# Performance work log

Measured on AMD Instinct MI355X. Metric: run time of the kernel, lower is better.

## Reference

```python
import jax, jax.numpy as jnp
import numpy as np

NUM_INPUTS = 24
FACTOR = 16
VOCAB = 1_000_000
BATCH = 8192
PAIRS = NUM_INPUTS * (NUM_INPUTS - 1) // 2  # 276
HIDDEN = 64


def setup_inputs() -> dict:
    key = jax.random.key(0)
    ks = jax.random.split(key, 8)
    inputs = jax.random.randint(ks[0], (BATCH, NUM_INPUTS), 0, VOCAB)
    s = 0.01
    w = jax.random.normal(ks[1], (VOCAB, 1), dtype=jnp.float32) * s
    v = jax.random.normal(ks[2], (VOCAB, FACTOR), dtype=jnp.float32) * s
    b = jnp.zeros((1,), dtype=jnp.float32)
    W1 = jax.random.normal(ks[3], (PAIRS, 2 * FACTOR, HIDDEN), dtype=jnp.float32) * s
    b1 = jnp.zeros((PAIRS, HIDDEN), dtype=jnp.float32)
    W2 = jax.random.normal(ks[4], (PAIRS, HIDDEN, 1), dtype=jnp.float32) * s
    b2 = jnp.zeros((PAIRS, 1), dtype=jnp.float32)
    return {"inputs": inputs, "w": w, "v": v, "b": b,
            "W1": W1, "b1": b1, "W2": W2, "b2": b2}


def reference(inputs, w, v, b, W1, b1, W2, b2):
    # pair index lists (i < j) -- static
    ii, jj = np.triu_indices(NUM_INPUTS, k=1)
    ii = jnp.asarray(ii)
    jj = jnp.asarray(jj)

    # linear term: sum of 1-dim embeddings over fields
    xw = w[inputs]                      # [B, n, 1]
    l = jnp.sum(xw, axis=(1, 2))        # [B]

    # pairwise concat of factor embeddings
    xv = v[inputs]                      # [B, n, f]
    prods = jnp.concatenate([xv[:, ii, :], xv[:, jj, :]], axis=-1)  # [B, P, 2f]
    prods = jnp.transpose(prods, (1, 0, 2))                         # [P, B, 2f]

    # per-pair stacked MLP: layer 0 relu, layer 1 identity
    h = jax.nn.relu(jnp.einsum('pbi,pio->pbo', prods, W1) + b1[:, None, :])  # [P, B, H]
    out = jnp.einsum('pbi,pio->pbo', h, W2) + b2[:, None, :]                  # [P, B, 1]

    # sum over concat of pair outputs == sum over pairs and last dim
    p = jnp.sum(out, axis=(0, 2))       # [B]

    logits = l + p + b[0]
    return jax.nn.sigmoid(logits)
```

## Files before the change

### kernel.cpp

```cpp
#include <hip/hip_runtime.h>
#include <hip/hip_bf16.h>
#include <math.h>

#define BATCH   8192
#define NFIELD  24
#define FAC     16
#define PAIRS   276
#define NSETS   24
#define SETLEN  12
#define NBB     (BATCH / 64)

typedef __attribute__((ext_vector_type(8))) __bf16 bf16x8;
typedef __attribute__((ext_vector_type(4))) float f32x4;

#define XVT_OFF   0
#define COMBO_OFF 6291456
#define PART_OFF  (COMBO_OFF + 1285632)
#define WVAL_OFF  (PART_OFF + 786432)
#define CONST_OFF (WVAL_OFF + 786432)

__global__ void prep_all(const int* __restrict__ inputs,
                         const float* __restrict__ v,
                         const float* __restrict__ w,
                         const float* __restrict__ W1,
                         const float* __restrict__ W2,
                         const float* __restrict__ b1,
                         const float* __restrict__ b2,
                         const float* __restrict__ bsc,
                         __hip_bfloat16* __restrict__ xvT,
                         char* __restrict__ combo,
                         float* __restrict__ wval,
                         float* __restrict__ consts) {
    __shared__ float red[256];
    int blk = blockIdx.x;
    if (blk < 768) {
        int t = blk * 256 + threadIdx.x;
        int field = t >> 13;
        int b = t & 8191;
        int idx = inputs[b * NFIELD + field];
        const float4* src = (const float4*)(v + (long)idx * FAC);
        union { __hip_bfloat16 h[16]; uint4 u[2]; } tmp;
        float4 a0 = src[0], a1 = src[1], a2 = src[2], a3 = src[3];
        tmp.h[0]  = __float2bfloat16(a0.x); tmp.h[1]  = __float2bfloat16(a0.y);
        tmp.h[2]  = __float2bfloat16(a0.z); tmp.h[3]  = __float2bfloat16(a0.w);
        tmp.h[4]  = __float2bfloat16(a1.x); tmp.h[5]  = __float2bfloat16(a1.y);
        tmp.h[6]  = __float2bfloat16(a1.z); tmp.h[7]  = __float2bfloat16(a1.w);
        tmp.h[8]  = __float2bfloat16(a2.x); tmp.h[9]  = __float2bfloat16(a2.y);
        tmp.h[10] = __float2bfloat16(a2.z); tmp.h[11] = __float2bfloat16(a2.w);
        tmp.h[12] = __float2bfloat16(a3.x); tmp.h[13] = __float2bfloat16(a3.y);
        tmp.h[14] = __float2bfloat16(a3.z); tmp.h[15] = __float2bfloat16(a3.w);
        int bb = b >> 6, row = b & 63;
        __hip_bfloat16* base = xvT + (long)bb * 24576 + field * 1024 + row * 8;
        *(uint4*)base         = tmp.u[0];
        *(uint4*)(base + 512) = tmp.u[1];
        wval[field * BATCH + b] = w[idx];
    } else {
        int wb = blk - 768;
        int t = wb * 256 + threadIdx.x;
        int p = t >> 6;
        int L = t & 63;
        int q = L >> 4, c = L & 15;
        char* base = combo + (long)p * 4608;
        union { __hip_bfloat16 h[8]; uint4 u; } buf;
#pragma unroll
        for (int tt = 0; tt < 4; ++tt) {
#pragma unroll
            for (int jj = 0; jj < 8; ++jj)
                buf.h[jj] = __float2bfloat16(W1[p * 2048 + (q * 8 + jj) * 64 + tt * 16 + c]);
            *(uint4*)(base + 512 + tt * 1024 + L * 16) = buf.u;
        }
        if (L < 16) {
            float4 bv = {b1[p * 64 + L], b1[p * 64 + 16 + L], b1[p * 64 + 32 + L], b1[p * 64 + 48 + L]};
            *(float4*)(base + L * 16) = bv;
            float4 wv = {W2[p * 64 + L], W2[p * 64 + 16 + L], W2[p * 64 + 32 + L], W2[p * 64 + 48 + L]};
            *(float4*)(base + 256 + L * 16) = wv;
        }
        if (wb == 1) {
            uint4 z = {0, 0, 0, 0};
            for (int k = threadIdx.x; k < 576; k += 256)
                *(uint4*)(combo + (long)PAIRS * 4608 + k * 16) = z;
        }
        if (wb == 0) {
            float s = 0.f;
            for (int k = threadIdx.x; k < PAIRS; k += 256) s += b2[k];
            red[threadIdx.x] = s;
            __syncthreads();
            for (int off = 128; off > 0; off >>= 1) {
                if (threadIdx.x < off) red[threadIdx.x] += red[threadIdx.x + off];
                __syncthreads();
            }
            if (threadIdx.x == 0) consts[0] = red[0] + bsc[0];
        }
    }
}

struct Pkg {
    f32x4 cb0, cb1, cb2, cb3;
    float4 mw;
    bf16x8 f0, f1, f2, f3;
};

__device__ __forceinline__ Pkg load_pkg(const char* p, int mcol, int l16) {
    Pkg k;
    float4 tb = *(const float4*)(p + mcol);
    k.cb0 = (f32x4){tb.x, tb.x, tb.x, tb.x};
    k.cb1 = (f32x4){tb.y, tb.y, tb.y, tb.y};
    k.cb2 = (f32x4){tb.z, tb.z, tb.z, tb.z};
    k.cb3 = (f32x4){tb.w, tb.w, tb.w, tb.w};
    k.mw = *(const float4*)(p + 256 + mcol);
    k.f0 = *(const bf16x8*)(p + 512  + l16);
    k.f1 = *(const bf16x8*)(p + 1536 + l16);
    k.f2 = *(const bf16x8*)(p + 2560 + l16);
    k.f3 = *(const bf16x8*)(p + 3584 + l16);
    return k;
}

#define PKGCOMP(P)                                                            \
    {                                                                         \
        int fso = ((quad < 2) ? i : j) * 1088;                                \
        const f32x4 z4 = {0.f, 0.f, 0.f, 0.f};                                \
        _Pragma("unroll")                                                     \
        for (int t = 0; t < 4; ++t) {                                         \
            bf16x8 af = *(const bf16x8*)(xv_s + fso + abase + t * 128);       \
            f32x4 c0 = __builtin_amdgcn_mfma_f32_16x16x32_bf16(af, P.f0, P.cb0, 0, 0, 0); \
            f32x4 c1 = __builtin_amdgcn_mfma_f32_16x16x32_bf16(af, P.f1, P.cb1, 0, 0, 0); \
            f32x4 c2 = __builtin_amdgcn_mfma_f32_16x16x32_bf16(af, P.f2, P.cb2, 0, 0, 0); \
            f32x4 c3 = __builtin_amdgcn_mfma_f32_16x16x32_bf16(af, P.f3, P.cb3, 0, 0, 0); \
            acc[t] = acc[t] + __builtin_elementwise_max(c0, z4) * P.mw.x;     \
            acc[t] = acc[t] + __builtin_elementwise_max(c1, z4) * P.mw.y;     \
            acc[t] = acc[t] + __builtin_elementwise_max(c2, z4) * P.mw.z;     \
            acc[t] = acc[t] + __builtin_elementwise_max(c3, z4) * P.mw.w;     \
        }                                                                     \
        ++j;                                                                  \
        if (j == NFIELD) { ++i; j = i + 1; }                                  \
    }

__global__ __launch_bounds__(256, 3) void ffm_main(
        const __hip_bfloat16* __restrict__ xvT,
        const char* __restrict__ combo,
        float* __restrict__ partial) {
    __shared__ __align__(16) __hip_bfloat16 xv_s[24 * 1088];

    int tid  = threadIdx.x;
    int bb   = blockIdx.x & (NBB - 1);
    int pg   = blockIdx.x >> 7;
    int lane = tid & 63;
    int wave = tid >> 6;
    int col  = lane & 15;
    int quad = lane >> 4;

    {
        const uint4* src = (const uint4*)(xvT + (long)bb * 24576);
#pragma unroll
        for (int it = 0; it < 12; ++it) {
            int ch = tid + it * 256;
            *(uint4*)(xv_s + ch * 8 + (ch >> 6) * 32) = src[ch];
        }
    }
    __syncthreads();

    int setid = pg * 4 + wave;
    f32x4 acc[4];
#pragma unroll
    for (int t = 0; t < 4; ++t) acc[t] = (f32x4){0.f, 0.f, 0.f, 0.f};

    const int abase = (quad & 1) * 544 + col * 8;
    const int mcol  = col * 16;
    const int l16   = lane * 16;

    if (setid < 23) {
        int p0 = setid * SETLEN;
        int i = 0, rem = p0;
        while (rem >= NFIELD - 1 - i) { rem -= NFIELD - 1 - i; ++i; }
        int j = i + 1 + rem;

        const char* wp = combo + (long)p0 * 4608;
        Pkg A = load_pkg(wp, mcol, l16);
        Pkg B = load_pkg(wp + 4608, mcol, l16);

#pragma unroll 2
        for (int k = 0; k < SETLEN; k += 2) {
            PKGCOMP(A)
            A = load_pkg(wp + 2 * 4608, mcol, l16);
            PKGCOMP(B)
            B = load_pkg(wp + 3 * 4608, mcol, l16);
            wp += 2 * 4608;
        }
    }

#pragma unroll
    for (int m = 1; m < 16; m <<= 1) {
#pragma unroll
        for (int t = 0; t < 4; ++t) {
#pragma unroll
            for (int r = 0; r < 4; ++r) acc[t][r] += __shfl_xor(acc[t][r], m, 64);
        }
    }
    if (col == 0) {
#pragma unroll
        for (int t = 0; t < 4; ++t) {
            f32x4 o = acc[t];
            *(f32x4*)&partial[setid * BATCH + bb * 64 + t * 16 + quad * 4] = o;
        }
    }
}

__global__ void finalize(const float* __restrict__ wval,
                         const float* __restrict__ consts,
                         const float* __restrict__ partial,
                         float* __restrict__ out) {
    int b = blockIdx.x * 256 + threadIdx.x;
    float s = consts[0];
#pragma unroll
    for (int f = 0; f < NFIELD; ++f) s += wval[f * BATCH + b];
#pragma unroll
    for (int g = 0; g < NSETS; ++g) s += partial[g * BATCH + b];
    out[b] = 1.0f / (1.0f + expf(-s));
}

extern "C" void kernel_launch(void* const* d_in, const int* in_sizes, int n_in,
                              void* d_out, int out_size, void* d_ws, size_t ws_size,
                              hipStream_t stream) {
    const int*   inputs = (const int*)d_in[0];
    const float* w      = (const float*)d_in[1];
    const float* v      = (const float*)d_in[2];
    const float* bsc    = (const float*)d_in[3];
    const float* W1     = (const float*)d_in[4];
    const float* b1     = (const float*)d_in[5];
    const float* W2     = (const float*)d_in[6];
    const float* b2     = (const float*)d_in[7];
    float* out = (float*)d_out;

    char* ws = (char*)d_ws;
    __hip_bfloat16* xvT = (__hip_bfloat16*)(ws + XVT_OFF);
    char*  combo   = ws + COMBO_OFF;
    float* partial = (float*)(ws + PART_OFF);
    float* wval    = (float*)(ws + WVAL_OFF);
    float* consts  = (float*)(ws + CONST_OFF);

    prep_all<<<768 + 69, 256, 0, stream>>>(inputs, v, w, W1, W2, b1, b2, bsc,
                                           xvT, combo, wval, consts);
    ffm_main<<<NBB * 6, 256, 0, stream>>>(xvT, combo, partial);
    finalize<<<BATCH / 256, 256, 0, stream>>>(wval, consts, partial, out);
}
```

Measured before the change: 136.5 us.

## Fuse prep, main and finalize into one cooperative kernel with grid syncs

Merges the three launches (gather/repack, per-pair MLP MFMA kernel, finalize) into a single cooperative kernel of 768 blocks that separates the phases with grid-wide syncs. The goal is to remove launch gaps and kernel-boundary drain between stages. The grid must fit co-resident (768 blocks at 3 per CU on 256 CUs). If the cooperative launch fails, the code falls back to the original three kernels. Grid syncs add their own barrier cost, and block-level load imbalance in the gather phase now stalls the whole grid.

```diff
diff --git a/kernel.cpp b/kernel.cpp
--- a/kernel.cpp
+++ b/kernel.cpp
@@ -1,6 +1,9 @@
 #include <hip/hip_runtime.h>
+#include <hip/hip_cooperative_groups.h>
 #include <hip/hip_bf16.h>
 #include <math.h>
+
+namespace cg = cooperative_groups;
 
 #define BATCH   8192
 #define NFIELD  24
@@ -19,79 +22,72 @@
 #define WVAL_OFF  (PART_OFF + 786432)
 #define CONST_OFF (WVAL_OFF + 786432)
 
-__global__ void prep_all(const int* __restrict__ inputs,
-                         const float* __restrict__ v,
-                         const float* __restrict__ w,
-                         const float* __restrict__ W1,
-                         const float* __restrict__ W2,
-                         const float* __restrict__ b1,
-                         const float* __restrict__ b2,
-                         const float* __restrict__ bsc,
-                         __hip_bfloat16* __restrict__ xvT,
-                         char* __restrict__ combo,
-                         float* __restrict__ wval,
-                         float* __restrict__ consts) {
-    __shared__ float red[256];
-    int blk = blockIdx.x;
-    if (blk < 768) {
-        int t = blk * 256 + threadIdx.x;
-        int field = t >> 13;
-        int b = t & 8191;
-        int idx = inputs[b * NFIELD + field];
-        const float4* src = (const float4*)(v + (long)idx * FAC);
-        union { __hip_bfloat16 h[16]; uint4 u[2]; } tmp;
-        float4 a0 = src[0], a1 = src[1], a2 = src[2], a3 = src[3];
-        tmp.h[0]  = __float2bfloat16(a0.x); tmp.h[1]  = __float2bfloat16(a0.y);
-        tmp.h[2]  = __float2bfloat16(a0.z); tmp.h[3]  = __float2bfloat16(a0.w);
-        tmp.h[4]  = __float2bfloat16(a1.x); tmp.h[5]  = __float2bfloat16(a1.y);
-        tmp.h[6]  = __float2bfloat16(a1.z); tmp.h[7]  = __float2bfloat16(a1.w);
-        tmp.h[8]  = __float2bfloat16(a2.x); tmp.h[9]  = __float2bfloat16(a2.y);
-        tmp.h[10] = __float2bfloat16(a2.z); tmp.h[11] = __float2bfloat16(a2.w);
-        tmp.h[12] = __float2bfloat16(a3.x); tmp.h[13] = __float2bfloat16(a3.y);
-        tmp.h[14] = __float2bfloat16(a3.z); tmp.h[15] = __float2bfloat16(a3.w);
-        int bb = b >> 6, row = b & 63;
-        __hip_bfloat16* base = xvT + (long)bb * 24576 + field * 1024 + row * 8;
-        *(uint4*)base         = tmp.u[0];
-        *(uint4*)(base + 512) = tmp.u[1];
-        wval[field * BATCH + b] = w[idx];
-    } else {
-        int wb = blk - 768;
-        int t = wb * 256 + threadIdx.x;
-        int p = t >> 6;
-        int L = t & 63;
-        int q = L >> 4, c = L & 15;
-        char* base = combo + (long)p * 4608;
-        union { __hip_bfloat16 h[8]; uint4 u; } buf;
-#pragma unroll
-        for (int tt = 0; tt < 4; ++tt) {
-#pragma unroll
-            for (int jj = 0; jj < 8; ++jj)
-                buf.h[jj] = __float2bfloat16(W1[p * 2048 + (q * 8 + jj) * 64 + tt * 16 + c]);
-            *(uint4*)(base + 512 + tt * 1024 + L * 16) = buf.u;
-        }
-        if (L < 16) {
-            float4 bv = {b1[p * 64 + L], b1[p * 64 + 16 + L], b1[p * 64 + 32 + L], b1[p * 64 + 48 + L]};
-            *(float4*)(base + L * 16) = bv;
-            float4 wv = {W2[p * 64 + L], W2[p * 64 + 16 + L], W2[p * 64 + 32 + L], W2[p * 64 + 48 + L]};
-            *(float4*)(base + 256 + L * 16) = wv;
-        }
-        if (wb == 1) {
-            uint4 z = {0, 0, 0, 0};
-            for (int k = threadIdx.x; k < 576; k += 256)
-                *(uint4*)(combo + (long)PAIRS * 4608 + k * 16) = z;
-        }
-        if (wb == 0) {
-            float s = 0.f;
-            for (int k = threadIdx.x; k < PAIRS; k += 256) s += b2[k];
-            red[threadIdx.x] = s;
-            __syncthreads();
-            for (int off = 128; off > 0; off >>= 1) {
-                if (threadIdx.x < off) red[threadIdx.x] += red[threadIdx.x + off];
-                __syncthreads();
-            }
-            if (threadIdx.x == 0) consts[0] = red[0] + bsc[0];
-        }
-    }
+
+__device__ __forceinline__ void do_gather(int blk, int tid,
+        const int* __restrict__ inputs, const float* __restrict__ v,
+        const float* __restrict__ w,
+        __hip_bfloat16* __restrict__ xvT, float* __restrict__ wval) {
+    int t = blk * 256 + tid;
+    int field = t >> 13;
+    int b = t & 8191;
+    int idx = inputs[b * NFIELD + field];
+    const float4* src = (const float4*)(v + (long)idx * FAC);
+    union { __hip_bfloat16 h[16]; uint4 u[2]; } tmp;
+    float4 a0 = src[0], a1 = src[1], a2 = src[2], a3 = src[3];
+    tmp.h[0]  = __float2bfloat16(a0.x); tmp.h[1]  = __float2bfloat16(a0.y);
+    tmp.h[2]  = __float2bfloat16(a0.z); tmp.h[3]  = __float2bfloat16(a0.w);
+    tmp.h[4]  = __float2bfloat16(a1.x); tmp.h[5]  = __float2bfloat16(a1.y);
+    tmp.h[6]  = __float2bfloat16(a1.z); tmp.h[7]  = __float2bfloat16(a1.w);
+    tmp.h[8]  = __float2bfloat16(a2.x); tmp.h[9]  = __float2bfloat16(a2.y);
+    tmp.h[10] = __float2bfloat16(a2.z); tmp.h[11] = __float2bfloat16(a2.w);
+    tmp.h[12] = __float2bfloat16(a3.x); tmp.h[13] = __float2bfloat16(a3.y);
+    tmp.h[14] = __float2bfloat16(a3.z); tmp.h[15] = __float2bfloat16(a3.w);
+    int bb = b >> 6, row = b & 63;
+    __hip_bfloat16* base = xvT + (long)bb * 24576 + field * 1024 + row * 8;
+    *(uint4*)base         = tmp.u[0];
+    *(uint4*)(base + 512) = tmp.u[1];
+    wval[field * BATCH + b] = w[idx];
+}
+
+__device__ __forceinline__ void do_repack(int p, int L,
+        const float* __restrict__ W1, const float* __restrict__ W2,
+        const float* __restrict__ b1, char* __restrict__ combo) {
+    int q = L >> 4, c = L & 15;
+    char* base = combo + (long)p * 4608;
+    union { __hip_bfloat16 h[8]; uint4 u; } buf;
+#pragma unroll
+    for (int tt = 0; tt < 4; ++tt) {
+#pragma unroll
+        for (int jj = 0; jj < 8; ++jj)
+            buf.h[jj] = __float2bfloat16(W1[p * 2048 + (q * 8 + jj) * 64 + tt * 16 + c]);
+        *(uint4*)(base + 512 + tt * 1024 + L * 16) = buf.u;
+    }
+    if (L < 16) {
+        float4 bv = {b1[p * 64 + L], b1[p * 64 + 16 + L], b1[p * 64 + 32 + L], b1[p * 64 + 48 + L]};
+        *(float4*)(base + L * 16) = bv;
+        float4 wv = {W2[p * 64 + L], W2[p * 64 + 16 + L], W2[p * 64 + 32 + L], W2[p * 64 + 48 + L]};
+        *(float4*)(base + 256 + L * 16) = wv;
+    }
+}
+
+__device__ __forceinline__ void do_padzero(int tid, char* __restrict__ combo) {
+    uint4 z = {0, 0, 0, 0};
+    for (int k = tid; k < 576; k += 256)
+        *(uint4*)(combo + (long)PAIRS * 4608 + k * 16) = z;
+}
+
+__device__ __forceinline__ void do_b2sum(int tid, float* red,
+        const float* __restrict__ b2, const float* __restrict__ bsc,
+        float* __restrict__ consts) {
+    float s = 0.f;
+    for (int k = tid; k < PAIRS; k += 256) s += b2[k];
+    red[tid] = s;
+    __syncthreads();
+    for (int off = 128; off > 0; off >>= 1) {
+        if (tid < off) red[tid] += red[tid + off];
+        __syncthreads();
+    }
+    if (tid == 0) consts[0] = red[0] + bsc[0];
 }
 
 struct Pkg {
@@ -135,15 +131,13 @@
         if (j == NFIELD) { ++i; j = i + 1; }                                  \
     }
 
-__global__ __launch_bounds__(256, 3) void ffm_main(
+__device__ __forceinline__ void do_main(int blk, int tid,
+        __hip_bfloat16* xv_s,
         const __hip_bfloat16* __restrict__ xvT,
         const char* __restrict__ combo,
         float* __restrict__ partial) {
-    __shared__ __align__(16) __hip_bfloat16 xv_s[24 * 1088];
-
-    int tid  = threadIdx.x;
-    int bb   = blockIdx.x & (NBB - 1);
-    int pg   = blockIdx.x >> 7;
+    int bb   = blk & (NBB - 1);
+    int pg   = blk >> 7;
     int lane = tid & 63;
     int wave = tid >> 6;
     int col  = lane & 15;
@@ -205,17 +199,92 @@
     }
 }
 
+__device__ __forceinline__ void do_finalize(int b,
+        const float* __restrict__ wval, const float* __restrict__ consts,
+        const float* __restrict__ partial, float* __restrict__ out) {
+    float s = consts[0];
+#pragma unroll
+    for (int f = 0; f < NFIELD; ++f) s += wval[f * BATCH + b];
+#pragma unroll
+    for (int g = 0; g < NSETS; ++g) s += partial[g * BATCH + b];
+    out[b] = 1.0f / (1.0f + expf(-s));
+}
+
+__global__ __launch_bounds__(256, 3) void ffm_fused(
+        const int* __restrict__ inputs,
+        const float* __restrict__ v,
+        const float* __restrict__ w,
+        const float* __restrict__ W1,
+        const float* __restrict__ W2,
+        const float* __restrict__ b1,
+        const float* __restrict__ b2,
+        const float* __restrict__ bsc,
+        __hip_bfloat16* __restrict__ xvT,
+        char* __restrict__ combo,
+        float* __restrict__ wval,
+        float* __restrict__ consts,
+        float* __restrict__ partial,
+        float* __restrict__ out) {
+    __shared__ __align__(16) __hip_bfloat16 xv_s[24 * 1088];
+
+    cg::grid_group grid = cg::this_grid();
+    const int tid = threadIdx.x;
+    const int blk = blockIdx.x;
+
+    do_gather(blk, tid, inputs, v, w, xvT, wval);
+    if (blk < PAIRS) {
+        if (tid < 64) do_repack(blk, tid, W1, W2, b1, combo);
+    } else if (blk == PAIRS) {
+        do_padzero(tid, combo);
+    } else if (blk == PAIRS + 1) {
+        do_b2sum(tid, (float*)xv_s, b2, bsc, consts);
+    }
+    grid.sync();
+
+    do_main(blk, tid, xv_s, xvT, combo, partial);
+    grid.sync();
+
+    if (blk < BATCH / 256) do_finalize(blk * 256 + tid, wval, consts, partial, out);
+}
+
+__global__ void prep_all(const int* __restrict__ inputs,
+                         const float* __restrict__ v,
+                         const float* __restrict__ w,
+                         const float* __restrict__ W1,
+                         const float* __restrict__ W2,
+                         const float* __restrict__ b1,
+                         const float* __restrict__ b2,
+                         const float* __restrict__ bsc,
+                         __hip_bfloat16* __restrict__ xvT,
+                         char* __restrict__ combo,
+                         float* __restrict__ wval,
+                         float* __restrict__ consts) {
+    __shared__ float red[256];
+    int blk = blockIdx.x;
+    if (blk < 768) {
+        do_gather(blk, threadIdx.x, inputs, v, w, xvT, wval);
+    } else {
+        int wb = blk - 768;
+        int t = wb * 256 + threadIdx.x;
+        do_repack(t >> 6, t & 63, W1, W2, b1, combo);
+        if (wb == 1) do_padzero(threadIdx.x, combo);
+        if (wb == 0) do_b2sum(threadIdx.x, red, b2, bsc, consts);
+    }
+}
+
+__global__ __launch_bounds__(256, 3) void ffm_main(
+        const __hip_bfloat16* __restrict__ xvT,
+        const char* __restrict__ combo,
+        float* __restrict__ partial) {
+    __shared__ __align__(16) __hip_bfloat16 xv_s[24 * 1088];
+    do_main(blockIdx.x, threadIdx.x, xv_s, xvT, combo, partial);
+}
+
 __global__ void finalize(const float* __restrict__ wval,
                          const float* __restrict__ consts,
                          const float* __restrict__ partial,
                          float* __restrict__ out) {
-    int b = blockIdx.x * 256 + threadIdx.x;
-    float s = consts[0];
-#pragma unroll
-    for (int f = 0; f < NFIELD; ++f) s += wval[f * BATCH + b];
-#pragma unroll
-    for (int g = 0; g < NSETS; ++g) s += partial[g * BATCH + b];
-    out[b] = 1.0f / (1.0f + expf(-s));
+    do_finalize(blockIdx.x * 256 + threadIdx.x, wval, consts, partial, out);
 }
 
 extern "C" void kernel_launch(void* const* d_in, const int* in_sizes, int n_in,
@@ -238,8 +307,16 @@
     float* wval    = (float*)(ws + WVAL_OFF);
     float* consts  = (float*)(ws + CONST_OFF);
 
-    prep_all<<<768 + 69, 256, 0, stream>>>(inputs, v, w, W1, W2, b1, b2, bsc,
-                                           xvT, combo, wval, consts);
-    ffm_main<<<NBB * 6, 256, 0, stream>>>(xvT, combo, partial);
-    finalize<<<BATCH / 256, 256, 0, stream>>>(wval, consts, partial, out);
-}
+    void* args[] = {(void*)&inputs, (void*)&v, (void*)&w, (void*)&W1,
+                    (void*)&W2, (void*)&b1, (void*)&b2, (void*)&bsc,
+                    (void*)&xvT, (void*)&combo, (void*)&wval, (void*)&consts,
+                    (void*)&partial, (void*)&out};
+    hipError_t err = hipLaunchCooperativeKernel(ffm_fused, dim3(768), dim3(256),
+                                                args, 0u, stream);
+    if (err != hipSuccess) {
+        prep_all<<<768 + 69, 256, 0, stream>>>(inputs, v, w, W1, W2, b1, b2, bsc,
+                                               xvT, combo, wval, consts);
+        ffm_main<<<NBB * 6, 256, 0, stream>>>(xvT, combo, partial);
+        finalize<<<BATCH / 256, 256, 0, stream>>>(wval, consts, partial, out);
+    }
+}
```

Result: slower. 318.3 us (+133.3%).

## Fuse finalize into main kernel via last-block-done atomic counter

Applied to the files above, without the earlier changes.

Removes the separate finalize launch. Each main block increments a per-batch-block counter after writing its partial sums, and the sixth (last) block for that batch tile reduces the wval and partial rows and writes the sigmoid output. Counters are zeroed in the prep kernel. This saves one kernel launch and its gap, at the cost of a threadfence, an atomic and a tail reduction in the main kernel.

```diff
diff --git a/kernel.cpp b/kernel.cpp
--- a/kernel.cpp
+++ b/kernel.cpp
@@ -18,6 +18,75 @@
 #define PART_OFF  (COMBO_OFF + 1285632)
 #define WVAL_OFF  (PART_OFF + 786432)
 #define CONST_OFF (WVAL_OFF + 786432)
+#define CNT_OFF   (CONST_OFF + 256)
+
+
+__device__ __forceinline__ void do_gather(int blk, int tid,
+        const int* __restrict__ inputs, const float* __restrict__ v,
+        const float* __restrict__ w,
+        __hip_bfloat16* __restrict__ xvT, float* __restrict__ wval) {
+    int t = blk * 256 + tid;
+    int field = t >> 13;
+    int b = t & 8191;
+    int idx = inputs[b * NFIELD + field];
+    const float4* src = (const float4*)(v + (long)idx * FAC);
+    union { __hip_bfloat16 h[16]; uint4 u[2]; } tmp;
+    float4 a0 = src[0], a1 = src[1], a2 = src[2], a3 = src[3];
+    tmp.h[0]  = __float2bfloat16(a0.x); tmp.h[1]  = __float2bfloat16(a0.y);
+    tmp.h[2]  = __float2bfloat16(a0.z); tmp.h[3]  = __float2bfloat16(a0.w);
+    tmp.h[4]  = __float2bfloat16(a1.x); tmp.h[5]  = __float2bfloat16(a1.y);
+    tmp.h[6]  = __float2bfloat16(a1.z); tmp.h[7]  = __float2bfloat16(a1.w);
+    tmp.h[8]  = __float2bfloat16(a2.x); tmp.h[9]  = __float2bfloat16(a2.y);
+    tmp.h[10] = __float2bfloat16(a2.z); tmp.h[11] = __float2bfloat16(a2.w);
+    tmp.h[12] = __float2bfloat16(a3.x); tmp.h[13] = __float2bfloat16(a3.y);
+    tmp.h[14] = __float2bfloat16(a3.z); tmp.h[15] = __float2bfloat16(a3.w);
+    int bb = b >> 6, row = b & 63;
+    __hip_bfloat16* base = xvT + (long)bb * 24576 + field * 1024 + row * 8;
+    *(uint4*)base         = tmp.u[0];
+    *(uint4*)(base + 512) = tmp.u[1];
+    wval[field * BATCH + b] = w[idx];
+}
+
+__device__ __forceinline__ void do_repack(int p, int L,
+        const float* __restrict__ W1, const float* __restrict__ W2,
+        const float* __restrict__ b1, char* __restrict__ combo) {
+    int q = L >> 4, c = L & 15;
+    char* base = combo + (long)p * 4608;
+    union { __hip_bfloat16 h[8]; uint4 u; } buf;
+#pragma unroll
+    for (int tt = 0; tt < 4; ++tt) {
+#pragma unroll
+        for (int jj = 0; jj < 8; ++jj)
+            buf.h[jj] = __float2bfloat16(W1[p * 2048 + (q * 8 + jj) * 64 + tt * 16 + c]);
+        *(uint4*)(base + 512 + tt * 1024 + L * 16) = buf.u;
+    }
+    if (L < 16) {
+        float4 bv = {b1[p * 64 + L], b1[p * 64 + 16 + L], b1[p * 64 + 32 + L], b1[p * 64 + 48 + L]};
+        *(float4*)(base + L * 16) = bv;
+        float4 wv = {W2[p * 64 + L], W2[p * 64 + 16 + L], W2[p * 64 + 32 + L], W2[p * 64 + 48 + L]};
+        *(float4*)(base + 256 + L * 16) = wv;
+    }
+}
+
+__device__ __forceinline__ void do_padzero(int tid, char* __restrict__ combo) {
+    uint4 z = {0, 0, 0, 0};
+    for (int k = tid; k < 576; k += 256)
+        *(uint4*)(combo + (long)PAIRS * 4608 + k * 16) = z;
+}
+
+__device__ __forceinline__ void do_b2sum(int tid, float* red,
+        const float* __restrict__ b2, const float* __restrict__ bsc,
+        float* __restrict__ consts) {
+    float s = 0.f;
+    for (int k = tid; k < PAIRS; k += 256) s += b2[k];
+    red[tid] = s;
+    __syncthreads();
+    for (int off = 128; off > 0; off >>= 1) {
+        if (tid < off) red[tid] += red[tid + off];
+        __syncthreads();
+    }
+    if (tid == 0) consts[0] = red[0] + bsc[0];
+}
 
 __global__ void prep_all(const int* __restrict__ inputs,
                          const float* __restrict__ v,
@@ -30,67 +99,19 @@
                          __hip_bfloat16* __restrict__ xvT,
                          char* __restrict__ combo,
                          float* __restrict__ wval,
-                         float* __restrict__ consts) {
+                         float* __restrict__ consts,
+                         int* __restrict__ cnt) {
     __shared__ float red[256];
     int blk = blockIdx.x;
     if (blk < 768) {
-        int t = blk * 256 + threadIdx.x;
-        int field = t >> 13;
-        int b = t & 8191;
-        int idx = inputs[b * NFIELD + field];
-        const float4* src = (const float4*)(v + (long)idx * FAC);
-        union { __hip_bfloat16 h[16]; uint4 u[2]; } tmp;
-        float4 a0 = src[0], a1 = src[1], a2 = src[2], a3 = src[3];
-        tmp.h[0]  = __float2bfloat16(a0.x); tmp.h[1]  = __float2bfloat16(a0.y);
-        tmp.h[2]  = __float2bfloat16(a0.z); tmp.h[3]  = __float2bfloat16(a0.w);
-        tmp.h[4]  = __float2bfloat16(a1.x); tmp.h[5]  = __float2bfloat16(a1.y);
-        tmp.h[6]  = __float2bfloat16(a1.z); tmp.h[7]  = __float2bfloat16(a1.w);
-        tmp.h[8]  = __float2bfloat16(a2.x); tmp.h[9]  = __float2bfloat16(a2.y);
-        tmp.h[10] = __float2bfloat16(a2.z); tmp.h[11] = __float2bfloat16(a2.w);
-        tmp.h[12] = __float2bfloat16(a3.x); tmp.h[13] = __float2bfloat16(a3.y);
-        tmp.h[14] = __float2bfloat16(a3.z); tmp.h[15] = __float2bfloat16(a3.w);
-        int bb = b >> 6, row = b & 63;
-        __hip_bfloat16* base = xvT + (long)bb * 24576 + field * 1024 + row * 8;
-        *(uint4*)base         = tmp.u[0];
-        *(uint4*)(base + 512) = tmp.u[1];
-        wval[field * BATCH + b] = w[idx];
+        do_gather(blk, threadIdx.x, inputs, v, w, xvT, wval);
     } else {
         int wb = blk - 768;
         int t = wb * 256 + threadIdx.x;
-        int p = t >> 6;
-        int L = t & 63;
-        int q = L >> 4, c = L & 15;
-        char* base = combo + (long)p * 4608;
-        union { __hip_bfloat16 h[8]; uint4 u; } buf;
-#pragma unroll
-        for (int tt = 0; tt < 4; ++tt) {
-#pragma unroll
-            for (int jj = 0; jj < 8; ++jj)
-                buf.h[jj] = __float2bfloat16(W1[p * 2048 + (q * 8 + jj) * 64 + tt * 16 + c]);
-            *(uint4*)(base + 512 + tt * 1024 + L * 16) = buf.u;
-        }
-        if (L < 16) {
-            float4 bv = {b1[p * 64 + L], b1[p * 64 + 16 + L], b1[p * 64 + 32 + L], b1[p * 64 + 48 + L]};
-            *(float4*)(base + L * 16) = bv;
-            float4 wv = {W2[p * 64 + L], W2[p * 64 + 16 + L], W2[p * 64 + 32 + L], W2[p * 64 + 48 + L]};
-            *(float4*)(base + 256 + L * 16) = wv;
-        }
-        if (wb == 1) {
-            uint4 z = {0, 0, 0, 0};
-            for (int k = threadIdx.x; k < 576; k += 256)
-                *(uint4*)(combo + (long)PAIRS * 4608 + k * 16) = z;
-        }
-        if (wb == 0) {
-            float s = 0.f;
-            for (int k = threadIdx.x; k < PAIRS; k += 256) s += b2[k];
-            red[threadIdx.x] = s;
-            __syncthreads();
-            for (int off = 128; off > 0; off >>= 1) {
-                if (threadIdx.x < off) red[threadIdx.x] += red[threadIdx.x + off];
-                __syncthreads();
-            }
-            if (threadIdx.x == 0) consts[0] = red[0] + bsc[0];
-        }
+        do_repack(t >> 6, t & 63, W1, W2, b1, combo);
+        if (wb == 1) do_padzero(threadIdx.x, combo);
+        if (wb == 2 && threadIdx.x < NBB) cnt[threadIdx.x] = 0;
+        if (wb == 0) do_b2sum(threadIdx.x, red, b2, bsc, consts);
     }
 }
 
@@ -135,15 +156,13 @@
         if (j == NFIELD) { ++i; j = i + 1; }                                  \
     }
 
-__global__ __launch_bounds__(256, 3) void ffm_main(
+__device__ __forceinline__ void do_main(int blk, int tid,
+        __hip_bfloat16* xv_s,
         const __hip_bfloat16* __restrict__ xvT,
         const char* __restrict__ combo,
         float* __restrict__ partial) {
-    __shared__ __align__(16) __hip_bfloat16 xv_s[24 * 1088];
-
-    int tid  = threadIdx.x;
-    int bb   = blockIdx.x & (NBB - 1);
-    int pg   = blockIdx.x >> 7;
+    int bb   = blk & (NBB - 1);
+    int pg   = blk >> 7;
     int lane = tid & 63;
     int wave = tid >> 6;
     int col  = lane & 15;
@@ -205,17 +224,43 @@
     }
 }
 
-__global__ void finalize(const float* __restrict__ wval,
-                         const float* __restrict__ consts,
-                         const float* __restrict__ partial,
-                         float* __restrict__ out) {
-    int b = blockIdx.x * 256 + threadIdx.x;
-    float s = consts[0];
-#pragma unroll
-    for (int f = 0; f < NFIELD; ++f) s += wval[f * BATCH + b];
-#pragma unroll
-    for (int g = 0; g < NSETS; ++g) s += partial[g * BATCH + b];
-    out[b] = 1.0f / (1.0f + expf(-s));
+__global__ __launch_bounds__(256, 3) void ffm_main(
+        const __hip_bfloat16* __restrict__ xvT,
+        const char* __restrict__ combo,
+        const float* __restrict__ wval,
+        const float* __restrict__ consts,
+        float* __restrict__ partial,
+        int* __restrict__ cnt,
+        float* __restrict__ out) {
+    __shared__ __align__(16) __hip_bfloat16 xv_s[24 * 1088];
+    __shared__ int win_s;
+
+    int tid = threadIdx.x;
+    int bb  = blockIdx.x & (NBB - 1);
+
+    do_main(blockIdx.x, tid, xv_s, xvT, combo, partial);
+
+    __threadfence();
+    __syncthreads();
+    if (tid == 0) win_s = (atomicAdd(&cnt[bb], 1) == 5);
+    __syncthreads();
+    if (win_s) {
+        __threadfence();
+        float* red = (float*)xv_s;
+        int r = tid & 63, grp = tid >> 6;
+        int base = bb * 64 + r;
+        float s = 0.f;
+#pragma unroll
+        for (int k = 0; k < 6; ++k) s += wval[(grp * 6 + k) * BATCH + base];
+#pragma unroll
+        for (int k = 0; k < 6; ++k) s += partial[(grp * 6 + k) * BATCH + base];
+        red[grp * 64 + r] = s;
+        __syncthreads();
+        if (tid < 64) {
+            float t2 = consts[0] + red[tid] + red[64 + tid] + red[128 + tid] + red[192 + tid];
+            out[bb * 64 + tid] = 1.0f / (1.0f + expf(-t2));
+        }
+    }
 }
 
 extern "C" void kernel_launch(void* const* d_in, const int* in_sizes, int n_in,
@@ -237,9 +282,10 @@
     float* partial = (float*)(ws + PART_OFF);
     float* wval    = (float*)(ws + WVAL_OFF);
     float* consts  = (float*)(ws + CONST_OFF);
+    int*   cnt     = (int*)(ws + CNT_OFF);
 
     prep_all<<<768 + 69, 256, 0, stream>>>(inputs, v, w, W1, W2, b1, b2, bsc,
-                                           xvT, combo, wval, consts);
-    ffm_main<<<NBB * 6, 256, 0, stream>>>(xvT, combo, partial);
-    finalize<<<BATCH / 256, 256, 0, stream>>>(wval, consts, partial, out);
-}
+                                           xvT, combo, wval, consts, cnt);
+    ffm_main<<<NBB * 6, 256, 0, stream>>>(xvT, combo, wval, consts,
+                                          partial, cnt, out);
+}
```

After: 192.4 us. +41.0%, slower.

## Fuse embedding gather into main kernel and drop xvT staging buffer

Applied to the files above, without the earlier changes.

The main kernel now gathers the 24 field embeddings for its 64-row batch tile straight from the vocabulary table, converts them to bf16 and writes them into shared memory, so the separate gather pass that wrote and re-read a 6 MB transposed buffer is gone. The first pair-weight packages are loaded before the gather so their latency overlaps it. The linear-term sum is reduced in-block by the pg==0 blocks and written as one value per row, which shrinks the finalize reads. In exchange each batch tile's gather is repeated by all 6 pair-group blocks, so random reads from the embedding table go up sixfold.

```diff
diff --git a/kernel.cpp b/kernel.cpp
--- a/kernel.cpp
+++ b/kernel.cpp
@@ -13,86 +13,62 @@
 typedef __attribute__((ext_vector_type(8))) __bf16 bf16x8;
 typedef __attribute__((ext_vector_type(4))) float f32x4;
 
-#define XVT_OFF   0
-#define COMBO_OFF 6291456
-#define PART_OFF  (COMBO_OFF + 1285632)
-#define WVAL_OFF  (PART_OFF + 786432)
-#define CONST_OFF (WVAL_OFF + 786432)
-
-__global__ void prep_all(const int* __restrict__ inputs,
-                         const float* __restrict__ v,
-                         const float* __restrict__ w,
-                         const float* __restrict__ W1,
-                         const float* __restrict__ W2,
-                         const float* __restrict__ b1,
-                         const float* __restrict__ b2,
-                         const float* __restrict__ bsc,
-                         __hip_bfloat16* __restrict__ xvT,
-                         char* __restrict__ combo,
-                         float* __restrict__ wval,
-                         float* __restrict__ consts) {
+#define COMBO_OFF 0
+#define PART_OFF  1285632
+#define WSUM_OFF  (PART_OFF + 786432)
+#define CONST_OFF (WSUM_OFF + 32768)
+
+
+__device__ __forceinline__ void do_repack(int p, int L,
+        const float* __restrict__ W1, const float* __restrict__ W2,
+        const float* __restrict__ b1, char* __restrict__ combo) {
+    int q = L >> 4, c = L & 15;
+    char* base = combo + (long)p * 4608;
+    union { __hip_bfloat16 h[8]; uint4 u; } buf;
+#pragma unroll
+    for (int tt = 0; tt < 4; ++tt) {
+#pragma unroll
+        for (int jj = 0; jj < 8; ++jj)
+            buf.h[jj] = __float2bfloat16(W1[p * 2048 + (q * 8 + jj) * 64 + tt * 16 + c]);
+        *(uint4*)(base + 512 + tt * 1024 + L * 16) = buf.u;
+    }
+    if (L < 16) {
+        float4 bv = {b1[p * 64 + L], b1[p * 64 + 16 + L], b1[p * 64 + 32 + L], b1[p * 64 + 48 + L]};
+        *(float4*)(base + L * 16) = bv;
+        float4 wv = {W2[p * 64 + L], W2[p * 64 + 16 + L], W2[p * 64 + 32 + L], W2[p * 64 + 48 + L]};
+        *(float4*)(base + 256 + L * 16) = wv;
+    }
+}
+
+__global__ void prep_w(const float* __restrict__ W1,
+                       const float* __restrict__ W2,
+                       const float* __restrict__ b1,
+                       const float* __restrict__ b2,
+                       const float* __restrict__ bsc,
+                       char* __restrict__ combo,
+                       float* __restrict__ consts) {
     __shared__ float red[256];
     int blk = blockIdx.x;
-    if (blk < 768) {
-        int t = blk * 256 + threadIdx.x;
-        int field = t >> 13;
-        int b = t & 8191;
-        int idx = inputs[b * NFIELD + field];
-        const float4* src = (const float4*)(v + (long)idx * FAC);
-        union { __hip_bfloat16 h[16]; uint4 u[2]; } tmp;
-        float4 a0 = src[0], a1 = src[1], a2 = src[2], a3 = src[3];
-        tmp.h[0]  = __float2bfloat16(a0.x); tmp.h[1]  = __float2bfloat16(a0.y);
-        tmp.h[2]  = __float2bfloat16(a0.z); tmp.h[3]  = __float2bfloat16(a0.w);
-        tmp.h[4]  = __float2bfloat16(a1.x); tmp.h[5]  = __float2bfloat16(a1.y);
-        tmp.h[6]  = __float2bfloat16(a1.z); tmp.h[7]  = __float2bfloat16(a1.w);
-        tmp.h[8]  = __float2bfloat16(a2.x); tmp.h[9]  = __float2bfloat16(a2.y);
-        tmp.h[10] = __float2bfloat16(a2.z); tmp.h[11] = __float2bfloat16(a2.w);
-        tmp.h[12] = __float2bfloat16(a3.x); tmp.h[13] = __float2bfloat16(a3.y);
-        tmp.h[14] = __float2bfloat16(a3.z); tmp.h[15] = __float2bfloat16(a3.w);
-        int bb = b >> 6, row = b & 63;
-        __hip_bfloat16* base = xvT + (long)bb * 24576 + field * 1024 + row * 8;
-        *(uint4*)base         = tmp.u[0];
-        *(uint4*)(base + 512) = tmp.u[1];
-        wval[field * BATCH + b] = w[idx];
-    } else {
-        int wb = blk - 768;
-        int t = wb * 256 + threadIdx.x;
-        int p = t >> 6;
-        int L = t & 63;
-        int q = L >> 4, c = L & 15;
-        char* base = combo + (long)p * 4608;
-        union { __hip_bfloat16 h[8]; uint4 u; } buf;
-#pragma unroll
-        for (int tt = 0; tt < 4; ++tt) {
-#pragma unroll
-            for (int jj = 0; jj < 8; ++jj)
-                buf.h[jj] = __float2bfloat16(W1[p * 2048 + (q * 8 + jj) * 64 + tt * 16 + c]);
-            *(uint4*)(base + 512 + tt * 1024 + L * 16) = buf.u;
-        }
-        if (L < 16) {
-            float4 bv = {b1[p * 64 + L], b1[p * 64 + 16 + L], b1[p * 64 + 32 + L], b1[p * 64 + 48 + L]};
-            *(float4*)(base + L * 16) = bv;
-            float4 wv = {W2[p * 64 + L], W2[p * 64 + 16 + L], W2[p * 64 + 32 + L], W2[p * 64 + 48 + L]};
-            *(float4*)(base + 256 + L * 16) = wv;
-        }
-        if (wb == 1) {
-            uint4 z = {0, 0, 0, 0};
-            for (int k = threadIdx.x; k < 576; k += 256)
-                *(uint4*)(combo + (long)PAIRS * 4608 + k * 16) = z;
-        }
-        if (wb == 0) {
-            float s = 0.f;
-            for (int k = threadIdx.x; k < PAIRS; k += 256) s += b2[k];
-            red[threadIdx.x] = s;
+    int t = blk * 256 + threadIdx.x;
+    do_repack(t >> 6, t & 63, W1, W2, b1, combo);
+    if (blk == 1) {
+        uint4 z = {0, 0, 0, 0};
+        for (int k = threadIdx.x; k < 576; k += 256)
+            *(uint4*)(combo + (long)PAIRS * 4608 + k * 16) = z;
+    }
+    if (blk == 0) {
+        float s = 0.f;
+        for (int k = threadIdx.x; k < PAIRS; k += 256) s += b2[k];
+        red[threadIdx.x] = s;
+        __syncthreads();
+        for (int off = 128; off > 0; off >>= 1) {
+            if (threadIdx.x < off) red[threadIdx.x] += red[threadIdx.x + off];
             __syncthreads();
-            for (int off = 128; off > 0; off >>= 1) {
-                if (threadIdx.x < off) red[threadIdx.x] += red[threadIdx.x + off];
-                __syncthreads();
-            }
-            if (threadIdx.x == 0) consts[0] = red[0] + bsc[0];
-        }
-    }
-}
+        }
+        if (threadIdx.x == 0) consts[0] = red[0] + bsc[0];
+    }
+}
+
 
 struct Pkg {
     f32x4 cb0, cb1, cb2, cb3;
@@ -136,10 +112,14 @@
     }
 
 __global__ __launch_bounds__(256, 3) void ffm_main(
-        const __hip_bfloat16* __restrict__ xvT,
-        const char* __restrict__ combo,
+        const int*   __restrict__ inputs,
+        const float* __restrict__ v,
+        const float* __restrict__ w,
+        const char*  __restrict__ combo,
+        float* __restrict__ wsum,
         float* __restrict__ partial) {
     __shared__ __align__(16) __hip_bfloat16 xv_s[24 * 1088];
+    __shared__ float wred[256];
 
     int tid  = threadIdx.x;
     int bb   = blockIdx.x & (NBB - 1);
@@ -149,35 +129,63 @@
     int col  = lane & 15;
     int quad = lane >> 4;
 
-    {
-        const uint4* src = (const uint4*)(xvT + (long)bb * 24576);
-#pragma unroll
-        for (int it = 0; it < 12; ++it) {
-            int ch = tid + it * 256;
-            *(uint4*)(xv_s + ch * 8 + (ch >> 6) * 32) = src[ch];
-        }
-    }
-    __syncthreads();
-
-    int setid = pg * 4 + wave;
-    f32x4 acc[4];
-#pragma unroll
-    for (int t = 0; t < 4; ++t) acc[t] = (f32x4){0.f, 0.f, 0.f, 0.f};
-
     const int abase = (quad & 1) * 544 + col * 8;
     const int mcol  = col * 16;
     const int l16   = lane * 16;
 
-    if (setid < 23) {
+    int setid = pg * 4 + wave;
+    int i = 0, j = 1;
+    const char* wp = combo;
+    Pkg A, B;
+    bool active = (setid < 23);
+    if (active) {
         int p0 = setid * SETLEN;
-        int i = 0, rem = p0;
+        int rem = p0;
+        i = 0;
         while (rem >= NFIELD - 1 - i) { rem -= NFIELD - 1 - i; ++i; }
-        int j = i + 1 + rem;
-
-        const char* wp = combo + (long)p0 * 4608;
-        Pkg A = load_pkg(wp, mcol, l16);
-        Pkg B = load_pkg(wp + 4608, mcol, l16);
-
+        j = i + 1 + rem;
+        wp = combo + (long)p0 * 4608;
+        A = load_pkg(wp, mcol, l16);
+        B = load_pkg(wp + 4608, mcol, l16);
+    }
+
+    {
+        int row = tid & 63;
+        float ws_acc = 0.f;
+#pragma unroll
+        for (int k2 = 0; k2 < 6; ++k2) {
+            int u = k2 * 256 + tid;
+            int field = u >> 6;
+            int idx = inputs[(bb * 64 + row) * NFIELD + field];
+            const float4* src = (const float4*)(v + (long)idx * FAC);
+            union { __hip_bfloat16 h[16]; uint4 uu[2]; } tmp;
+            float4 a0 = src[0], a1 = src[1], a2 = src[2], a3 = src[3];
+            tmp.h[0]  = __float2bfloat16(a0.x); tmp.h[1]  = __float2bfloat16(a0.y);
+            tmp.h[2]  = __float2bfloat16(a0.z); tmp.h[3]  = __float2bfloat16(a0.w);
+            tmp.h[4]  = __float2bfloat16(a1.x); tmp.h[5]  = __float2bfloat16(a1.y);
+            tmp.h[6]  = __float2bfloat16(a1.z); tmp.h[7]  = __float2bfloat16(a1.w);
+            tmp.h[8]  = __float2bfloat16(a2.x); tmp.h[9]  = __float2bfloat16(a2.y);
+            tmp.h[10] = __float2bfloat16(a2.z); tmp.h[11] = __float2bfloat16(a2.w);
+            tmp.h[12] = __float2bfloat16(a3.x); tmp.h[13] = __float2bfloat16(a3.y);
+            tmp.h[14] = __float2bfloat16(a3.z); tmp.h[15] = __float2bfloat16(a3.w);
+            __hip_bfloat16* dst = xv_s + field * 1088 + row * 8;
+            *(uint4*)dst         = tmp.uu[0];
+            *(uint4*)(dst + 544) = tmp.uu[1];
+            if (pg == 0) ws_acc += w[idx];
+        }
+        if (pg == 0) wred[tid] = ws_acc;
+    }
+    __syncthreads();
+
+    if (pg == 0 && tid < 64) {
+        wsum[bb * 64 + tid] = wred[tid] + wred[64 + tid] + wred[128 + tid] + wred[192 + tid];
+    }
+
+    f32x4 acc[4];
+#pragma unroll
+    for (int t = 0; t < 4; ++t) acc[t] = (f32x4){0.f, 0.f, 0.f, 0.f};
+
+    if (active) {
 #pragma unroll 2
         for (int k = 0; k < SETLEN; k += 2) {
             PKGCOMP(A)
@@ -205,14 +213,12 @@
     }
 }
 
-__global__ void finalize(const float* __restrict__ wval,
+__global__ void finalize(const float* __restrict__ wsum,
                          const float* __restrict__ consts,
                          const float* __restrict__ partial,
                          float* __restrict__ out) {
     int b = blockIdx.x * 256 + threadIdx.x;
-    float s = consts[0];
-#pragma unroll
-    for (int f = 0; f < NFIELD; ++f) s += wval[f * BATCH + b];
+    float s = consts[0] + wsum[b];
 #pragma unroll
     for (int g = 0; g < NSETS; ++g) s += partial[g * BATCH + b];
     out[b] = 1.0f / (1.0f + expf(-s));
@@ -232,14 +238,12 @@
     float* out = (float*)d_out;
 
     char* ws = (char*)d_ws;
-    __hip_bfloat16* xvT = (__hip_bfloat16*)(ws + XVT_OFF);
     char*  combo   = ws + COMBO_OFF;
     float* partial = (float*)(ws + PART_OFF);
-    float* wval    = (float*)(ws + WVAL_OFF);
+    float* wsum    = (float*)(ws + WSUM_OFF);
     float* consts  = (float*)(ws + CONST_OFF);
 
-    prep_all<<<768 + 69, 256, 0, stream>>>(inputs, v, w, W1, W2, b1, b2, bsc,
-                                           xvT, combo, wval, consts);
-    ffm_main<<<NBB * 6, 256, 0, stream>>>(xvT, combo, partial);
-    finalize<<<BATCH / 256, 256, 0, stream>>>(wval, consts, partial, out);
-}
+    prep_w<<<69, 256, 0, stream>>>(W1, W2, b1, b2, bsc, combo, consts);
+    ffm_main<<<NBB * 6, 256, 0, stream>>>(inputs, v, w, combo, wsum, partial);
+    finalize<<<BATCH / 256, 256, 0, stream>>>(wsum, consts, partial, out);
+}
```

Measured after the change: 141.4 us. 1.04x slower.
